# Performance work log

Hardware: AMD Instinct MI355X
Metric: run time of the kernel (lower is better)

## Reference

```python
import jax, jax.numpy as jnp
import numpy as np
import math

N_HEADS = 12


def setup_inputs() -> dict:
    key = jax.random.key(0)
    ks = jax.random.split(key, 6)
    B, S, DIM = 4, 2048, 768
    h = jax.random.normal(ks[0], (B, S, DIM), dtype=jnp.float32)
    attn_mask = jnp.ones((B, 1, 1, S), dtype=jnp.int32)
    scale = 1.0 / math.sqrt(DIM)
    wq = jax.random.normal(ks[1], (DIM, DIM), dtype=jnp.float32) * scale
    wk = jax.random.normal(ks[2], (DIM, DIM), dtype=jnp.float32) * scale
    wv = jax.random.normal(ks[3], (DIM, DIM), dtype=jnp.float32) * scale
    wo = jax.random.normal(ks[4], (DIM, DIM), dtype=jnp.float32) * scale
    return {"h": h, "attn_mask": attn_mask, "wq": wq, "wk": wk, "wv": wv, "wo": wo}


def reference(h, attn_mask, wq, wk, wv, wo):
    B, S, dim = h.shape
    H = N_HEADS
    D = dim // H
    qk_scale = 1.0 / math.sqrt(D)
    # NOTE: original uses .view(B, H, S, D) on the [B, S, H*D] projection —
    # a raw reshape, NOT the usual (B,S,H,D)->(B,H,S,D) transpose. Reproduce exactly.
    hq = (h @ wq.T).reshape(B, H, S, D)
    hk = (h @ wk.T).reshape(B, H, S, D)
    hv = (h @ wv.T).reshape(B, H, S, D)
    scores = jnp.einsum("bhqd,bhkd->bhqk", hq, hk) * qk_scale  # [B,H,S,S]
    scores = jnp.where(attn_mask == 0, -jnp.inf, scores)
    attn = jax.nn.softmax(scores.astype(jnp.float32), axis=-1)
    ctx = jnp.einsum("bhqk,bhkd->bhqd", attn, hv)  # [B,H,S,D]
    # dropout is identity in eval mode
    ctx = ctx.reshape(B, S, H * D)
    return ctx @ wo.T
```

## Files before the change

kernel.cpp:

```cpp
#include <hip/hip_runtime.h>
#include <math.h>

typedef __bf16 bf16x8 __attribute__((ext_vector_type(8)));
typedef float  f32x4  __attribute__((ext_vector_type(4)));
typedef float  f32x16 __attribute__((ext_vector_type(16)));

#define MFMA16(a, b, c) __builtin_amdgcn_mfma_f32_16x16x32_bf16((a), (b), (c), 0, 0, 0)
#define MFMA32(a, b, c) __builtin_amdgcn_mfma_f32_32x32x16_bf16((a), (b), (c), 0, 0, 0)

__device__ __forceinline__ unsigned short f2bf(float f) {
    unsigned int u = __float_as_uint(f);
    u += 0x7fffu + ((u >> 16) & 1u);
    return (unsigned short)(u >> 16);
}

__device__ __forceinline__ void gll16(const unsigned short* g, unsigned short* l) {
    __builtin_amdgcn_global_load_lds(
        (const __attribute__((address_space(1))) unsigned int*)g,
        (__attribute__((address_space(3))) unsigned int*)l, 16, 0, 0);
}

__global__ __launch_bounds__(256) void convert_kernel(
    const float* __restrict__ h, const float* __restrict__ wq,
    const float* __restrict__ wk, const float* __restrict__ wv,
    const float* __restrict__ wo,
    unsigned short* __restrict__ hb, unsigned short* __restrict__ wb)
{
    const int NH4 = 1572864;
    const int NW4 = 147456;
    int i4 = blockIdx.x * 256 + threadIdx.x;
    const float4* src;
    unsigned short* dst;
    int off;
    float sc = 1.0f;
    if (i4 < NH4) {
        src = (const float4*)h; dst = hb; off = i4;
    } else {
        int j = i4 - NH4;
        int w = j / NW4;
        off = j - w * NW4;
        const float* s = (w == 0) ? wq : (w == 1) ? wk : (w == 2) ? wv : wo;
        if (w == 0) sc = 0.18033688011112042f;
        src = (const float4*)s;
        dst = wb + w * 589824;
    }
    float4 v = src[off];
    ushort4 o;
    o.x = f2bf(v.x * sc); o.y = f2bf(v.y * sc);
    o.z = f2bf(v.z * sc); o.w = f2bf(v.w * sc);
    ((ushort4*)dst)[off] = o;
}

template <typename OutT>
__global__ __launch_bounds__(256) void gemm_bt(
    const unsigned short* __restrict__ A,
    const unsigned short* __restrict__ Bm,
    OutT* __restrict__ C)
{
    constexpr int K = 768, N = 768;
    __shared__ unsigned short As[2][128 * 32];
    __shared__ unsigned short Bs[2][128 * 32];
    const unsigned short* Bz = Bm + (size_t)blockIdx.z * N * K;
    OutT* Cz = C + (size_t)blockIdx.z * 8192 * N;

    const int tid  = threadIdx.x;
    const int bm   = blockIdx.x * 128, bn = blockIdx.y * 128;
    const int wave = tid >> 6, lane = tid & 63;
    const int wm   = (wave & 1) * 64, wn = (wave >> 1) * 64;
    const int l16  = lane & 15, quad = lane >> 4;

    const int sr  = tid >> 2;
    const int sp8 = ((tid & 3) ^ (sr & 3)) * 8;
    const int slot8 = (quad ^ (l16 & 3)) * 8;

    auto stage = [&](int k0, int bi) {
        gll16(A  + (size_t)(bm + sr) * K      + k0 + sp8, As[bi] + tid * 8);
        gll16(A  + (size_t)(bm + 64 + sr) * K + k0 + sp8, As[bi] + 2048 + tid * 8);
        gll16(Bz + (size_t)(bn + sr) * K      + k0 + sp8, Bs[bi] + tid * 8);
        gll16(Bz + (size_t)(bn + 64 + sr) * K + k0 + sp8, Bs[bi] + 2048 + tid * 8);
    };

    f32x4 acc[4][4] = {};

    stage(0, 0);
    __syncthreads();

    for (int i = 0; i < 24; i++) {
        const int cur = i & 1;
        if (i < 23) stage((i + 1) * 32, cur ^ 1);

        bf16x8 af[4], bfv[4];
        #pragma unroll
        for (int ii = 0; ii < 4; ii++)
            af[ii] = *(const bf16x8*)(As[cur] + (wm + ii * 16 + l16) * 32 + slot8);
        #pragma unroll
        for (int jj = 0; jj < 4; jj++)
            bfv[jj] = *(const bf16x8*)(Bs[cur] + (wn + jj * 16 + l16) * 32 + slot8);
        #pragma unroll
        for (int ii = 0; ii < 4; ii++)
            #pragma unroll
            for (int jj = 0; jj < 4; jj++)
                acc[ii][jj] = MFMA16(af[ii], bfv[jj], acc[ii][jj]);

        __syncthreads();
    }

    #pragma unroll
    for (int ii = 0; ii < 4; ii++) {
        #pragma unroll
        for (int jj = 0; jj < 4; jj++) {
            int row0 = bm + wm + ii * 16 + quad * 4;
            int col  = bn + wn + jj * 16 + l16;
            #pragma unroll
            for (int r = 0; r < 4; r++) {
                float v = acc[ii][jj][r];
                size_t idx = (size_t)(row0 + r) * N + col;
                if constexpr (sizeof(OutT) == 2) Cz[idx] = f2bf(v);
                else                             Cz[idx] = v;
            }
        }
    }
}

__global__ __launch_bounds__(256) void vtrans_kernel(
    const unsigned short* __restrict__ Vg,
    unsigned short* __restrict__ vt)
{
    constexpr int LDT = 72;
    __shared__ unsigned short Ts[64 * LDT];
    const int b = blockIdx.z, hh = blockIdx.y, kp0 = blockIdx.x * 64;
    const int tid = threadIdx.x;
    const size_t boff = (size_t)b * (24576 * 64);
    const int rowV0 = hh * 2048 + kp0;

    #pragma unroll
    for (int rep = 0; rep < 2; rep++) {
        int idx = rep * 256 + tid;
        int r = idx >> 3, dp = (idx & 7) * 8;
        uint4 v = *(const uint4*)(Vg + boff + (size_t)(rowV0 + r) * 64 + dp);
        unsigned short tmp[8];
        *(uint4*)tmp = v;
        #pragma unroll
        for (int i = 0; i < 8; i++) Ts[(dp + i) * LDT + r] = tmp[i];
    }
    __syncthreads();
    unsigned short* vtb = vt + ((size_t)(b * 12 + hh)) * 64 * 2048;
    #pragma unroll
    for (int rep = 0; rep < 2; rep++) {
        int idx = rep * 256 + tid;
        int d = idx >> 3, kp = (idx & 7) * 8;
        uint4 v = *(const uint4*)(Ts + d * LDT + kp);
        *(uint4*)(vtb + (size_t)d * 2048 + kp0 + kp) = v;
    }
}

__global__ __launch_bounds__(256) void attn_kernel(
    const unsigned short* __restrict__ Qg,
    const unsigned short* __restrict__ Kg,
    const unsigned short* __restrict__ vt,
    const int* __restrict__ mask,
    unsigned short* __restrict__ Og)
{
    __shared__ unsigned short Ks[3 * 4096];
    __shared__ unsigned short Vs[3 * 4096];
    __shared__ unsigned long long msh[32];

    const int b = blockIdx.z, hh = blockIdx.y, qt = blockIdx.x;
    const int tid  = threadIdx.x;
    const int wave = tid >> 6, lane = tid & 63;
    const int c31  = lane & 31, h = lane >> 5;
    const size_t boff = (size_t)b * (24576 * 64);
    const int rowQ0 = hh * 2048 + qt * 128;
    const int rowK0 = hh * 2048;
    const unsigned short* vtg = vt + ((size_t)(b * 12 + hh)) * 64 * 2048;
    const int sw = c31 & 7;

    const int srow = tid >> 3;
    const int sch8 = ((tid & 7) ^ (srow & 7)) * 8;

    auto stageKV = [&](int kt, int bi) {
        #pragma unroll
        for (int i = 0; i < 2; i++) {
            int row = i * 32 + srow;
            gll16(Kg  + boff + (size_t)(rowK0 + kt * 64 + row) * 64 + sch8,
                  Ks + bi * 4096 + i * 2048 + tid * 8);
            gll16(vtg + (size_t)row * 2048 + kt * 64 + sch8,
                  Vs + bi * 4096 + i * 2048 + tid * 8);
        }
    };

    bf16x8 qf[4];
    {
        const unsigned short* qrow =
            Qg + boff + (size_t)(rowQ0 + wave * 32 + c31) * 64;
        #pragma unroll
        for (int c = 0; c < 4; c++)
            qf[c] = *(const bf16x8*)(qrow + (2 * c + h) * 8);
    }

    {
        const int4 a = *(const int4*)(mask + b * 2048 + tid * 8);
        const int4 c = *(const int4*)(mask + b * 2048 + tid * 8 + 4);
        unsigned char byte =
            (a.x != 0 ? 1u : 0u)       | (a.y != 0 ? 2u : 0u) |
            (a.z != 0 ? 4u : 0u)       | (a.w != 0 ? 8u : 0u) |
            (c.x != 0 ? 16u : 0u)      | (c.y != 0 ? 32u : 0u) |
            (c.z != 0 ? 64u : 0u)      | (c.w != 0 ? 128u : 0u);
        ((unsigned char*)msh)[tid] = byte;
    }
    __syncthreads();

    stageKV(0, 0);
    stageKV(1, 1);

    f32x16 acc[2] = {};
    f32x16 acc_l  = {};
    bf16x8 onesf;
    #pragma unroll
    for (int i = 0; i < 8; i++) onesf[i] = (__bf16)1.0f;

    int cur = 0;
    for (int kt = 0; kt < 32; kt++) {
        if (kt < 31) asm volatile("s_waitcnt vmcnt(4)\n\ts_barrier" ::: "memory");
        else         asm volatile("s_waitcnt vmcnt(0)\n\ts_barrier" ::: "memory");
        __builtin_amdgcn_sched_barrier(0);

        if (kt < 30) {
            int nb = cur + 2; if (nb >= 3) nb -= 3;
            stageKV(kt + 2, nb);
        }

        const unsigned long long am = msh[kt];
        const unsigned short* Kc = Ks + cur * 4096;
        const unsigned short* Vc = Vs + cur * 4096;

        f32x16 sT[2];
        #pragma unroll
        for (int t2 = 0; t2 < 2; t2++) {
            f32x16 z = {};
            #pragma unroll
            for (int c = 0; c < 4; c++) {
                int ch = (2 * c + h) ^ sw;
                bf16x8 kf = *(const bf16x8*)(Kc + (t2 * 32 + c31) * 64 + ch * 8);
                z = MFMA32(kf, qf[c], z);
            }
            sT[t2] = z;
        }

        unsigned int p01[2][4], p23[2][4];
        if (am == ~0ull) {
            #pragma unroll
            for (int t2 = 0; t2 < 2; t2++) {
                #pragma unroll
                for (int s = 0; s < 4; s++) {
                    float e0 = __builtin_amdgcn_exp2f(sT[t2][4*s+0]);
                    float e1 = __builtin_amdgcn_exp2f(sT[t2][4*s+1]);
                    float e2 = __builtin_amdgcn_exp2f(sT[t2][4*s+2]);
                    float e3 = __builtin_amdgcn_exp2f(sT[t2][4*s+3]);
                    asm("v_cvt_pk_bf16_f32 %0, %1, %2"
                        : "=v"(p01[t2][s]) : "v"(e0), "v"(e1));
                    asm("v_cvt_pk_bf16_f32 %0, %1, %2"
                        : "=v"(p23[t2][s]) : "v"(e2), "v"(e3));
                }
            }
        } else {
            #pragma unroll
            for (int t2 = 0; t2 < 2; t2++) {
                #pragma unroll
                for (int s = 0; s < 4; s++) {
                    unsigned int nib = (unsigned int)(am >> (t2 * 32 + 8 * s + 4 * h)) & 0xFu;
                    float e0 = __builtin_amdgcn_exp2f(sT[t2][4*s+0]);
                    float e1 = __builtin_amdgcn_exp2f(sT[t2][4*s+1]);
                    float e2 = __builtin_amdgcn_exp2f(sT[t2][4*s+2]);
                    float e3 = __builtin_amdgcn_exp2f(sT[t2][4*s+3]);
                    e0 = (nib & 1u) ? e0 : 0.f;
                    e1 = (nib & 2u) ? e1 : 0.f;
                    e2 = (nib & 4u) ? e2 : 0.f;
                    e3 = (nib & 8u) ? e3 : 0.f;
                    asm("v_cvt_pk_bf16_f32 %0, %1, %2"
                        : "=v"(p01[t2][s]) : "v"(e0), "v"(e1));
                    asm("v_cvt_pk_bf16_f32 %0, %1, %2"
                        : "=v"(p23[t2][s]) : "v"(e2), "v"(e3));
                }
            }
        }

        #pragma unroll
        for (int q = 0; q < 4; q++) {
            int t = q >> 1, p = q & 1;
            unsigned int a01 = p01[t][2 * p], b01 = p01[t][2 * p + 1];
            unsigned int a23 = p23[t][2 * p], b23 = p23[t][2 * p + 1];
            asm("v_permlane32_swap_b32 %0, %1" : "+v"(a01), "+v"(b01));
            asm("v_permlane32_swap_b32 %0, %1" : "+v"(a23), "+v"(b23));
            uint4 pfu;
            pfu.x = a01;
            pfu.y = a23;
            pfu.z = b01;
            pfu.w = b23;
            bf16x8 pf;
            __builtin_memcpy(&pf, &pfu, 16);
            #pragma unroll
            for (int nt = 0; nt < 2; nt++) {
                int ch = (2 * q + h) ^ sw;
                bf16x8 vf = *(const bf16x8*)(Vc + (nt * 32 + c31) * 64 + ch * 8);
                acc[nt] = MFMA32(pf, vf, acc[nt]);
            }
            acc_l = MFMA32(pf, onesf, acc_l);
        }

        cur = (cur == 2) ? 0 : cur + 1;
    }

    #pragma unroll
    for (int reg = 0; reg < 16; reg++) {
        int rowfn = (reg & 3) + 8 * (reg >> 2) + 4 * h;
        float li = __builtin_amdgcn_rcpf(acc_l[reg]);
        int row = rowQ0 + wave * 32 + rowfn;
        #pragma unroll
        for (int nt = 0; nt < 2; nt++)
            Og[boff + (size_t)row * 64 + nt * 32 + c31] = f2bf(acc[nt][reg] * li);
    }
}

extern "C" void kernel_launch(void* const* d_in, const int* in_sizes, int n_in,
                              void* d_out, int out_size, void* d_ws, size_t ws_size,
                              hipStream_t stream)
{
    const float* h    = (const float*)d_in[0];
    const int*   mask = (const int*)d_in[1];
    const float* wq   = (const float*)d_in[2];
    const float* wk   = (const float*)d_in[3];
    const float* wv   = (const float*)d_in[4];
    const float* wo   = (const float*)d_in[5];

    unsigned short* hb  = (unsigned short*)d_ws;
    unsigned short* wb  = hb + 6291456;
    unsigned short* qkv = wb + 4 * 589824;
    unsigned short* ctx = qkv + (size_t)3 * 6291456;

    convert_kernel<<<8448, 256, 0, stream>>>(h, wq, wk, wv, wo, hb, wb);
    gemm_bt<unsigned short><<<dim3(64, 6, 3), 256, 0, stream>>>(hb, wb, qkv);
    vtrans_kernel<<<dim3(32, 12, 4), 256, 0, stream>>>(qkv + (size_t)2 * 6291456, hb);
    attn_kernel<<<dim3(16, 12, 4), 256, 0, stream>>>(
        qkv, qkv + 6291456, hb, mask, ctx);
    gemm_bt<float><<<dim3(64, 6, 1), 256, 0, stream>>>(
        ctx, wb + (size_t)3 * 589824, (float*)d_out);
}
```

Before: 253.1 us.

## Halve attention KV tile to 32 keys and add MFMA priority hints

Shrinks each K/V stage from 64 to 32 keys. The triple-buffered LDS footprint halves, which may allow more resident blocks, and the main loop now runs 64 iterations. The V tile layout and swizzle are changed to 32-wide rows, and the mask is read as a 32-bit word per tile. s_setprio is raised around the MFMA sections so waves doing matrix work get issue priority. The cost is twice as many barriers and waitcnt points per block, with less work between them.

```diff
diff --git a/kernel.cpp b/kernel.cpp
--- a/kernel.cpp
+++ b/kernel.cpp
@@ -161,8 +161,8 @@
     const int* __restrict__ mask,
     unsigned short* __restrict__ Og)
 {
-    __shared__ unsigned short Ks[3 * 4096];
-    __shared__ unsigned short Vs[3 * 4096];
+    __shared__ unsigned short Ks[3 * 2048];
+    __shared__ unsigned short Vs[3 * 2048];
     __shared__ unsigned long long msh[32];
 
     const int b = blockIdx.z, hh = blockIdx.y, qt = blockIdx.x;
@@ -173,20 +173,19 @@
     const int rowQ0 = hh * 2048 + qt * 128;
     const int rowK0 = hh * 2048;
     const unsigned short* vtg = vt + ((size_t)(b * 12 + hh)) * 64 * 2048;
-    const int sw = c31 & 7;
-
-    const int srow = tid >> 3;
-    const int sch8 = ((tid & 7) ^ (srow & 7)) * 8;
+    const int swk = c31 & 7;
+    const int swv = c31 & 3;
+
+    const int srowK = tid >> 3;
+    const int schK  = ((tid & 7) ^ (srowK & 7)) * 8;
+    const int srowV = tid >> 2;
+    const int schV  = ((tid & 3) ^ (srowV & 3)) * 8;
 
     auto stageKV = [&](int kt, int bi) {
-        #pragma unroll
-        for (int i = 0; i < 2; i++) {
-            int row = i * 32 + srow;
-            gll16(Kg  + boff + (size_t)(rowK0 + kt * 64 + row) * 64 + sch8,
-                  Ks + bi * 4096 + i * 2048 + tid * 8);
-            gll16(vtg + (size_t)row * 2048 + kt * 64 + sch8,
-                  Vs + bi * 4096 + i * 2048 + tid * 8);
-        }
+        gll16(Kg  + boff + (size_t)(rowK0 + kt * 32 + srowK) * 64 + schK,
+              Ks + bi * 2048 + tid * 8);
+        gll16(vtg + (size_t)srowV * 2048 + kt * 32 + schV,
+              Vs + bi * 2048 + tid * 8);
     };
 
     bf16x8 qf[4];
@@ -220,76 +219,71 @@
     for (int i = 0; i < 8; i++) onesf[i] = (__bf16)1.0f;
 
     int cur = 0;
-    for (int kt = 0; kt < 32; kt++) {
-        if (kt < 31) asm volatile("s_waitcnt vmcnt(4)\n\ts_barrier" ::: "memory");
+    for (int kt = 0; kt < 64; kt++) {
+        if (kt < 63) asm volatile("s_waitcnt vmcnt(2)\n\ts_barrier" ::: "memory");
         else         asm volatile("s_waitcnt vmcnt(0)\n\ts_barrier" ::: "memory");
         __builtin_amdgcn_sched_barrier(0);
 
-        if (kt < 30) {
+        if (kt < 62) {
             int nb = cur + 2; if (nb >= 3) nb -= 3;
             stageKV(kt + 2, nb);
         }
 
-        const unsigned long long am = msh[kt];
-        const unsigned short* Kc = Ks + cur * 4096;
-        const unsigned short* Vc = Vs + cur * 4096;
-
-        f32x16 sT[2];
-        #pragma unroll
-        for (int t2 = 0; t2 < 2; t2++) {
+        const unsigned int am = ((const unsigned int*)msh)[kt];
+        const unsigned short* Kc = Ks + cur * 2048;
+        const unsigned short* Vc = Vs + cur * 2048;
+
+        f32x16 sT;
+        {
             f32x16 z = {};
+            __builtin_amdgcn_s_setprio(1);
             #pragma unroll
             for (int c = 0; c < 4; c++) {
-                int ch = (2 * c + h) ^ sw;
-                bf16x8 kf = *(const bf16x8*)(Kc + (t2 * 32 + c31) * 64 + ch * 8);
+                int ch = (2 * c + h) ^ swk;
+                bf16x8 kf = *(const bf16x8*)(Kc + c31 * 64 + ch * 8);
                 z = MFMA32(kf, qf[c], z);
             }
-            sT[t2] = z;
-        }
-
-        unsigned int p01[2][4], p23[2][4];
-        if (am == ~0ull) {
-            #pragma unroll
-            for (int t2 = 0; t2 < 2; t2++) {
-                #pragma unroll
-                for (int s = 0; s < 4; s++) {
-                    float e0 = __builtin_amdgcn_exp2f(sT[t2][4*s+0]);
-                    float e1 = __builtin_amdgcn_exp2f(sT[t2][4*s+1]);
-                    float e2 = __builtin_amdgcn_exp2f(sT[t2][4*s+2]);
-                    float e3 = __builtin_amdgcn_exp2f(sT[t2][4*s+3]);
-                    asm("v_cvt_pk_bf16_f32 %0, %1, %2"
-                        : "=v"(p01[t2][s]) : "v"(e0), "v"(e1));
-                    asm("v_cvt_pk_bf16_f32 %0, %1, %2"
-                        : "=v"(p23[t2][s]) : "v"(e2), "v"(e3));
-                }
+            __builtin_amdgcn_s_setprio(0);
+            sT = z;
+        }
+
+        unsigned int p01[4], p23[4];
+        if (am == 0xFFFFFFFFu) {
+            #pragma unroll
+            for (int s = 0; s < 4; s++) {
+                float e0 = __builtin_amdgcn_exp2f(sT[4*s+0]);
+                float e1 = __builtin_amdgcn_exp2f(sT[4*s+1]);
+                float e2 = __builtin_amdgcn_exp2f(sT[4*s+2]);
+                float e3 = __builtin_amdgcn_exp2f(sT[4*s+3]);
+                asm("v_cvt_pk_bf16_f32 %0, %1, %2"
+                    : "=v"(p01[s]) : "v"(e0), "v"(e1));
+                asm("v_cvt_pk_bf16_f32 %0, %1, %2"
+                    : "=v"(p23[s]) : "v"(e2), "v"(e3));
             }
         } else {
             #pragma unroll
-            for (int t2 = 0; t2 < 2; t2++) {
-                #pragma unroll
-                for (int s = 0; s < 4; s++) {
-                    unsigned int nib = (unsigned int)(am >> (t2 * 32 + 8 * s + 4 * h)) & 0xFu;
-                    float e0 = __builtin_amdgcn_exp2f(sT[t2][4*s+0]);
-                    float e1 = __builtin_amdgcn_exp2f(sT[t2][4*s+1]);
-                    float e2 = __builtin_amdgcn_exp2f(sT[t2][4*s+2]);
-                    float e3 = __builtin_amdgcn_exp2f(sT[t2][4*s+3]);
-                    e0 = (nib & 1u) ? e0 : 0.f;
-                    e1 = (nib & 2u) ? e1 : 0.f;
-                    e2 = (nib & 4u) ? e2 : 0.f;
-                    e3 = (nib & 8u) ? e3 : 0.f;
-                    asm("v_cvt_pk_bf16_f32 %0, %1, %2"
-                        : "=v"(p01[t2][s]) : "v"(e0), "v"(e1));
-                    asm("v_cvt_pk_bf16_f32 %0, %1, %2"
-                        : "=v"(p23[t2][s]) : "v"(e2), "v"(e3));
-                }
-            }
-        }
-
-        #pragma unroll
-        for (int q = 0; q < 4; q++) {
-            int t = q >> 1, p = q & 1;
-            unsigned int a01 = p01[t][2 * p], b01 = p01[t][2 * p + 1];
-            unsigned int a23 = p23[t][2 * p], b23 = p23[t][2 * p + 1];
+            for (int s = 0; s < 4; s++) {
+                unsigned int nib = (am >> (8 * s + 4 * h)) & 0xFu;
+                float e0 = __builtin_amdgcn_exp2f(sT[4*s+0]);
+                float e1 = __builtin_amdgcn_exp2f(sT[4*s+1]);
+                float e2 = __builtin_amdgcn_exp2f(sT[4*s+2]);
+                float e3 = __builtin_amdgcn_exp2f(sT[4*s+3]);
+                e0 = (nib & 1u) ? e0 : 0.f;
+                e1 = (nib & 2u) ? e1 : 0.f;
+                e2 = (nib & 4u) ? e2 : 0.f;
+                e3 = (nib & 8u) ? e3 : 0.f;
+                asm("v_cvt_pk_bf16_f32 %0, %1, %2"
+                    : "=v"(p01[s]) : "v"(e0), "v"(e1));
+                asm("v_cvt_pk_bf16_f32 %0, %1, %2"
+                    : "=v"(p23[s]) : "v"(e2), "v"(e3));
+            }
+        }
+
+        __builtin_amdgcn_s_setprio(1);
+        #pragma unroll
+        for (int kc = 0; kc < 2; kc++) {
+            unsigned int a01 = p01[2 * kc], b01 = p01[2 * kc + 1];
+            unsigned int a23 = p23[2 * kc], b23 = p23[2 * kc + 1];
             asm("v_permlane32_swap_b32 %0, %1" : "+v"(a01), "+v"(b01));
             asm("v_permlane32_swap_b32 %0, %1" : "+v"(a23), "+v"(b23));
             uint4 pfu;
@@ -301,12 +295,13 @@
             __builtin_memcpy(&pf, &pfu, 16);
             #pragma unroll
             for (int nt = 0; nt < 2; nt++) {
-                int ch = (2 * q + h) ^ sw;
-                bf16x8 vf = *(const bf16x8*)(Vc + (nt * 32 + c31) * 64 + ch * 8);
+                int chv = (2 * kc + h) ^ swv;
+                bf16x8 vf = *(const bf16x8*)(Vc + (nt * 32 + c31) * 32 + chv * 8);
                 acc[nt] = MFMA32(pf, vf, acc[nt]);
             }
             acc_l = MFMA32(pf, onesf, acc_l);
         }
+        __builtin_amdgcn_s_setprio(0);
 
         cur = (cur == 2) ? 0 : cur + 1;
     }
```

Result: faster. 244.3 us (-3.5%).
